# Performance work log

Measured on AMD Instinct MI355X. Metric: run time of the kernel, lower is better.

Reference implementation:

```python
import jax, jax.numpy as jnp
import numpy as np

UP = 4  # upsample factor of DispUpsampleBySlantedPlane


def _l1_warp_cost(fea_l, fea_r, disp):
    """Warp fea_r horizontally by disp (grid_sample bilinear, zeros padding,
    align_corners=True) and return per-pixel L1 distance over channels.
    fea_l, fea_r: [B, C, H, W]; disp: [B, H, W] -> returns [B, H, W]."""
    B, C, H, W = fea_l.shape
    x = jnp.arange(W, dtype=disp.dtype)
    xf = x[None, None, :] - disp              # sample position in right image
    x0 = jnp.floor(xf)
    w1 = xf - x0                              # weight for x0+1
    w0 = 1.0 - w1
    x0i = x0.astype(jnp.int32)
    x1i = x0i + 1
    v0 = ((x0i >= 0) & (x0i < W)).astype(fea_l.dtype)  # zeros padding masks
    v1 = ((x1i >= 0) & (x1i < W)).astype(fea_l.dtype)
    x0c = jnp.clip(x0i, 0, W - 1)
    x1c = jnp.clip(x1i, 0, W - 1)
    idx0 = jnp.broadcast_to(x0c[:, None, :, :], (B, C, H, W))
    idx1 = jnp.broadcast_to(x1c[:, None, :, :], (B, C, H, W))
    g0 = jnp.take_along_axis(fea_r, idx0, axis=3)
    g1 = jnp.take_along_axis(fea_r, idx1, axis=3)
    warped = g0 * (w0 * v0)[:, None] + g1 * (w1 * v1)[:, None]
    return jnp.sum(jnp.abs(fea_l - warped), axis=1)  # L1 over channels


def _tile_warping(tile_plane, fea_l, fea_r):
    B, C, H, W = fea_l.shape
    h, w = tile_plane.shape[2], tile_plane.shape[3]
    d = tile_plane[:, 0]   # [B, h, w]
    dx = tile_plane[:, 1]
    dy = tile_plane[:, 2]
    # slanted-plane offsets for the 4x4 sub-pixels, centered at (UP-1)/2 = 1.5
    off = jnp.arange(UP, dtype=fea_l.dtype) - (UP - 1) / 2.0
    outs = []
    for disp_d in (-1.0, 0.0, 1.0):
        # disp0[b, di, dj, th, tw] = (d + disp_d) + off[di]*dy + off[dj]*dx
        disp0 = ((d + disp_d)[:, None, None]
                 + off[None, :, None, None, None] * dy[:, None, None]
                 + off[None, None, :, None, None] * dx[:, None, None])
        # PixelShuffle(4): full-res disparity [B, H, W]
        disp_full = disp0.transpose(0, 3, 1, 4, 2).reshape(B, H, W)
        cv = _l1_warp_cost(fea_l, fea_r, disp_full)        # [B, H, W]
        # cv[:, :, i::4, j::4] for i,j in 0..3, concatenated on channel dim
        local = cv.reshape(B, h, UP, w, UP).transpose(0, 2, 4, 1, 3)
        outs.append(local.reshape(B, UP * UP, h, w))       # [B, 16, h, w]
    return jnp.concatenate(outs, axis=1)                   # [B, 48, h, w]


def setup_inputs() -> dict:
    key = jax.random.key(0)
    k1, k2, k3 = jax.random.split(key, 3)
    B, C, H, W = 4, 16, 512, 960
    h, w = H // UP, W // UP
    tile_plane = jax.random.normal(k1, (B, 3, h, w), dtype=jnp.float32)
    fea_l = jax.random.normal(k2, (B, C, H, W), dtype=jnp.float32)
    fea_r = jax.random.normal(k3, (B, C, H, W), dtype=jnp.float32)
    return {"tile_plane": tile_plane, "fea_l": fea_l, "fea_r": fea_r}


def reference(tile_plane, fea_l, fea_r):
    return _tile_warping(tile_plane, fea_l, fea_r)
```

## Files before the change

kernel.cpp:

```cpp
#include <hip/hip_runtime.h>


#define NB 4
#define NC 16
#define NH 512
#define NW 960
#define TH 128
#define TW 240
#define HW (NH * NW)
#define GUARD 16
#define CHUNK 8
#define CBUF (2 * GUARD + CHUNK * NW)

typedef const __attribute__((address_space(1))) unsigned int* gas_u32;
typedef __attribute__((address_space(3))) unsigned int* las_u32;

__device__ __forceinline__ void stage16(const float* g, float* l) {
    __builtin_amdgcn_global_load_lds((gas_u32)g, (las_u32)l, 16, 0, 0);
}

__global__ __launch_bounds__(960, 8) void tile_warp_kernel(
    const float* __restrict__ tp,
    const float* __restrict__ fl,
    const float* __restrict__ fr,
    float* __restrict__ out)
{
    const int u = threadIdx.x;
    const int Y = blockIdx.x;
    const int b = blockIdx.y;
    const int y = Y >> 2, i = Y & 3;
    const int T = u >> 2, j = u & 3;

    __shared__ float smem[2][CBUF];

    const float* frrow = fr + (size_t)(b * NC) * HW + (size_t)Y * NW;
    const float* flrow = fl + (size_t)(b * NC) * HW + (size_t)Y * NW + u;

    {
        const int s0 = u, s1 = u + 960;
        stage16(frrow + (s0 / 240) * HW + 4 * (s0 % 240), &smem[0][GUARD + 4 * s0]);
        stage16(frrow + (s1 / 240) * HW + 4 * (s1 % 240), &smem[0][GUARD + 4 * s1]);
    }

    const int tpb = (b * 3 * TH + y) * TW + T;
    const float d   = tp[tpb];
    const float dxv = tp[tpb + TH * TW];
    const float dyv = tp[tpb + 2 * TH * TW];
    const float base = d + ((float)i - 1.5f) * dyv + ((float)j - 1.5f) * dxv;
    const float xf  = (float)u - base;
    const float x0f = floorf(xf);
    const float w1  = xf - x0f;
    const float w0  = 1.0f - w1;
    const int   x0  = (int)x0f;
    const int   p   = x0 - 1;
    const int   p_cl = max(min(p, NW + 12), -GUARD);

    float w0k[3], w1k[3];
#pragma unroll
    for (int kk = 0; kk < 3; ++kk) {
        const int xa = p + 2 - kk;
        const int xb = p + 3 - kk;
        w0k[kk] = (xa >= 0 && xa < NW) ? w0 : 0.0f;
        w1k[kk] = (xb >= 0 && xb < NW) ? w1 : 0.0f;
    }
    float acc0 = 0.f, acc1 = 0.f, acc2 = 0.f;

    __syncthreads();

    {
        const float* frrow1 = frrow + CHUNK * HW;
        const int s0 = u, s1 = u + 960;
        stage16(frrow1 + (s0 / 240) * HW + 4 * (s0 % 240), &smem[1][GUARD + 4 * s0]);
        stage16(frrow1 + (s1 / 240) * HW + 4 * (s1 % 240), &smem[1][GUARD + 4 * s1]);
    }

    {
        float flv[CHUNK];
#pragma unroll
        for (int c = 0; c < CHUNK; ++c) flv[c] = flrow[c * HW];
#pragma unroll
        for (int c = 0; c < CHUNK; ++c) {
            const float* L = &smem[0][GUARD + c * NW + p_cl];
            const float m0 = L[0], m1 = L[1], m2 = L[2], m3 = L[3];
            const float wv0 = m2 * w0k[0] + m3 * w1k[0];
            const float wv1 = m1 * w0k[1] + m2 * w1k[1];
            const float wv2 = m0 * w0k[2] + m1 * w1k[2];
            acc0 += fabsf(flv[c] - wv0);
            acc1 += fabsf(flv[c] - wv1);
            acc2 += fabsf(flv[c] - wv2);
        }
    }

    __syncthreads();

    {
        float flv[CHUNK];
#pragma unroll
        for (int c = 0; c < CHUNK; ++c) flv[c] = flrow[(CHUNK + c) * HW];
#pragma unroll
        for (int c = 0; c < CHUNK; ++c) {
            const float* L = &smem[1][GUARD + c * NW + p_cl];
            const float m0 = L[0], m1 = L[1], m2 = L[2], m3 = L[3];
            const float wv0 = m2 * w0k[0] + m3 * w1k[0];
            const float wv1 = m1 * w0k[1] + m2 * w1k[1];
            const float wv2 = m0 * w0k[2] + m1 * w1k[2];
            acc0 += fabsf(flv[c] - wv0);
            acc1 += fabsf(flv[c] - wv1);
            acc2 += fabsf(flv[c] - wv2);
        }
    }

    const size_t obase = ((size_t)(b * 48 + i * 4 + j) * TH + y) * TW + T;
    out[obase]                        = acc0;
    out[obase + 16 * (size_t)TH * TW] = acc1;
    out[obase + 32 * (size_t)TH * TW] = acc2;
}

extern "C" void kernel_launch(void* const* d_in, const int* in_sizes, int n_in,
                              void* d_out, int out_size, void* d_ws, size_t ws_size,
                              hipStream_t stream) {
    const float* tp = (const float*)d_in[0];
    const float* fl = (const float*)d_in[1];
    const float* fr = (const float*)d_in[2];
    float* out = (float*)d_out;

    dim3 grid(NH, NB);
    dim3 block(960);
    tile_warp_kernel<<<grid, block, 0, stream>>>(tp, fl, fr, out);
}
```

Measured before the change: 272.1 us.

## Split rows into 256-wide segments with guarded LDS windows and global fallback

Each block now handles a 256-pixel segment of one row for all 16 channels, instead of a whole 960-pixel row in two 8-channel chunks. Only the segment plus a 16-pixel guard on each side is staged in LDS, all channels at once, so the mid-kernel barrier and double buffer go away. Pixels whose sample falls outside the window take a slow path that reads fr straight from global memory. This gives smaller blocks and less LDS per block, aiming at more occupancy and finer scheduling. The cost is redundant guard loads, a 4th segment that is mostly idle (1024 threads for 960 pixels), and a divergent fallback path when disparities are large.

```diff
diff --git a/kernel.cpp b/kernel.cpp
--- a/kernel.cpp
+++ b/kernel.cpp
@@ -8,9 +8,11 @@
 #define TH 128
 #define TW 240
 #define HW (NH * NW)
+#define SEG 256
 #define GUARD 16
-#define CHUNK 8
-#define CBUF (2 * GUARD + CHUNK * NW)
+#define WIN (SEG + 2 * GUARD)
+#define SLOTS (NC * WIN / 4)
+#define SLOTS_PER_CH (WIN / 4)
 
 typedef const __attribute__((address_space(1))) unsigned int* gas_u32;
 typedef __attribute__((address_space(3))) unsigned int* las_u32;
@@ -19,101 +21,112 @@
     __builtin_amdgcn_global_load_lds((gas_u32)g, (las_u32)l, 16, 0, 0);
 }
 
-__global__ __launch_bounds__(960, 8) void tile_warp_kernel(
+__global__ __launch_bounds__(256, 8) void tile_warp_kernel(
     const float* __restrict__ tp,
     const float* __restrict__ fl,
     const float* __restrict__ fr,
     float* __restrict__ out)
 {
-    const int u = threadIdx.x;
-    const int Y = blockIdx.x;
-    const int b = blockIdx.y;
-    const int y = Y >> 2, i = Y & 3;
-    const int T = u >> 2, j = u & 3;
+    const int t = threadIdx.x;
+    const int s = blockIdx.x;
+    const int Y = blockIdx.y;
+    const int b = blockIdx.z;
+    const int base = s * SEG;
+    const int X = base + t;
 
-    __shared__ float smem[2][CBUF];
+    __shared__ float lds[NC * WIN];
 
     const float* frrow = fr + (size_t)(b * NC) * HW + (size_t)Y * NW;
-    const float* flrow = fl + (size_t)(b * NC) * HW + (size_t)Y * NW + u;
 
-    {
-        const int s0 = u, s1 = u + 960;
-        stage16(frrow + (s0 / 240) * HW + 4 * (s0 % 240), &smem[0][GUARD + 4 * s0]);
-        stage16(frrow + (s1 / 240) * HW + 4 * (s1 % 240), &smem[0][GUARD + 4 * s1]);
+#pragma unroll
+    for (int k = 0; k < 4; ++k) {
+        const int slot = t + 256 * k;
+        const int c = slot / SLOTS_PER_CH;
+        const int off = slot - c * SLOTS_PER_CH;
+        int gx = base - GUARD + 4 * off;
+        gx = min(max(gx, 0), NW - 4);
+        stage16(frrow + (size_t)c * HW + gx, &lds[4 * slot]);
+    }
+    if (t < SLOTS - 1024) {
+        const int slot = t + 1024;
+        const int c = slot / SLOTS_PER_CH;
+        const int off = slot - c * SLOTS_PER_CH;
+        int gx = base - GUARD + 4 * off;
+        gx = min(max(gx, 0), NW - 4);
+        stage16(frrow + (size_t)c * HW + gx, &lds[4 * slot]);
     }
 
-    const int tpb = (b * 3 * TH + y) * TW + T;
+    const int y = Y >> 2, i = Y & 3;
+    const int j = X & 3;
+    const int T = X >> 2;
+    const int Tc = min(T, TW - 1);
+
+    const int tpb = (b * 3 * TH + y) * TW + Tc;
     const float d   = tp[tpb];
     const float dxv = tp[tpb + TH * TW];
     const float dyv = tp[tpb + 2 * TH * TW];
-    const float base = d + ((float)i - 1.5f) * dyv + ((float)j - 1.5f) * dxv;
-    const float xf  = (float)u - base;
+    const float disp = d + ((float)i - 1.5f) * dyv + ((float)j - 1.5f) * dxv;
+    const float xf  = (float)X - disp;
     const float x0f = floorf(xf);
     const float w1  = xf - x0f;
     const float w0  = 1.0f - w1;
     const int   x0  = (int)x0f;
     const int   p   = x0 - 1;
-    const int   p_cl = max(min(p, NW + 12), -GUARD);
+    const int   q   = p - base + GUARD;
+    const int   qc  = min(max(q, 0), WIN - 4);
+    const bool  spill = (q != qc) && (X < NW);
 
     float w0k[3], w1k[3];
 #pragma unroll
     for (int kk = 0; kk < 3; ++kk) {
         const int xa = p + 2 - kk;
-        const int xb = p + 3 - kk;
+        const int xb = xa + 1;
         w0k[kk] = (xa >= 0 && xa < NW) ? w0 : 0.0f;
         w1k[kk] = (xb >= 0 && xb < NW) ? w1 : 0.0f;
     }
-    float acc0 = 0.f, acc1 = 0.f, acc2 = 0.f;
+
+    const float* flp = fl + (size_t)(b * NC) * HW + (size_t)Y * NW + min(X, NW - 1);
 
     __syncthreads();
 
-    {
-        const float* frrow1 = frrow + CHUNK * HW;
-        const int s0 = u, s1 = u + 960;
-        stage16(frrow1 + (s0 / 240) * HW + 4 * (s0 % 240), &smem[1][GUARD + 4 * s0]);
-        stage16(frrow1 + (s1 / 240) * HW + 4 * (s1 % 240), &smem[1][GUARD + 4 * s1]);
-    }
-
-    {
-        float flv[CHUNK];
+    float a0 = 0.f, a1 = 0.f, a2 = 0.f;
 #pragma unroll
-        for (int c = 0; c < CHUNK; ++c) flv[c] = flrow[c * HW];
+    for (int g = 0; g < 4; ++g) {
+        float flv[4];
 #pragma unroll
-        for (int c = 0; c < CHUNK; ++c) {
-            const float* L = &smem[0][GUARD + c * NW + p_cl];
+        for (int cc = 0; cc < 4; ++cc) flv[cc] = flp[(size_t)(4 * g + cc) * HW];
+#pragma unroll
+        for (int cc = 0; cc < 4; ++cc) {
+            const float* L = &lds[(4 * g + cc) * WIN + qc];
             const float m0 = L[0], m1 = L[1], m2 = L[2], m3 = L[3];
-            const float wv0 = m2 * w0k[0] + m3 * w1k[0];
-            const float wv1 = m1 * w0k[1] + m2 * w1k[1];
-            const float wv2 = m0 * w0k[2] + m1 * w1k[2];
-            acc0 += fabsf(flv[c] - wv0);
-            acc1 += fabsf(flv[c] - wv1);
-            acc2 += fabsf(flv[c] - wv2);
+            a0 += fabsf(flv[cc] - (m2 * w0k[0] + m3 * w1k[0]));
+            a1 += fabsf(flv[cc] - (m1 * w0k[1] + m2 * w1k[1]));
+            a2 += fabsf(flv[cc] - (m0 * w0k[2] + m1 * w1k[2]));
         }
     }
 
-    __syncthreads();
-
-    {
-        float flv[CHUNK];
-#pragma unroll
-        for (int c = 0; c < CHUNK; ++c) flv[c] = flrow[(CHUNK + c) * HW];
-#pragma unroll
-        for (int c = 0; c < CHUNK; ++c) {
-            const float* L = &smem[1][GUARD + c * NW + p_cl];
-            const float m0 = L[0], m1 = L[1], m2 = L[2], m3 = L[3];
-            const float wv0 = m2 * w0k[0] + m3 * w1k[0];
-            const float wv1 = m1 * w0k[1] + m2 * w1k[1];
-            const float wv2 = m0 * w0k[2] + m1 * w1k[2];
-            acc0 += fabsf(flv[c] - wv0);
-            acc1 += fabsf(flv[c] - wv1);
-            acc2 += fabsf(flv[c] - wv2);
+    if (__builtin_expect(spill, 0)) {
+        a0 = a1 = a2 = 0.f;
+        const int t0 = min(max(p,     0), NW - 1);
+        const int t1 = min(max(p + 1, 0), NW - 1);
+        const int t2 = min(max(p + 2, 0), NW - 1);
+        const int t3 = min(max(p + 3, 0), NW - 1);
+        for (int c = 0; c < NC; ++c) {
+            const float* R = frrow + (size_t)c * HW;
+            const float m0 = R[t0], m1 = R[t1], m2 = R[t2], m3 = R[t3];
+            const float fv = flp[(size_t)c * HW];
+            a0 += fabsf(fv - (m2 * w0k[0] + m3 * w1k[0]));
+            a1 += fabsf(fv - (m1 * w0k[1] + m2 * w1k[1]));
+            a2 += fabsf(fv - (m0 * w0k[2] + m1 * w1k[2]));
         }
     }
 
-    const size_t obase = ((size_t)(b * 48 + i * 4 + j) * TH + y) * TW + T;
-    out[obase]                        = acc0;
-    out[obase + 16 * (size_t)TH * TW] = acc1;
-    out[obase + 32 * (size_t)TH * TW] = acc2;
+    if (X < NW) {
+        const size_t ob = ((size_t)(b * 48 + i * 4 + j) * TH + y) * TW + T;
+        out[ob]                        = a0;
+        out[ob + 16 * (size_t)TH * TW] = a1;
+        out[ob + 32 * (size_t)TH * TW] = a2;
+    }
 }
 
 extern "C" void kernel_launch(void* const* d_in, const int* in_sizes, int n_in,
@@ -124,7 +137,7 @@
     const float* fr = (const float*)d_in[2];
     float* out = (float*)d_out;
 
-    dim3 grid(NH, NB);
-    dim3 block(960);
+    dim3 grid(4, NH, NB);
+    dim3 block(256);
     tile_warp_kernel<<<grid, block, 0, stream>>>(tp, fl, fr, out);
 }
```

Result: no change. 274.2 us (+0.7%).
